# Kernel optimization log

Measured on AMD Instinct MI355X. Metric: run time of the kernel, lower is better.

The kernel has to match this reference:

```python
import jax, jax.numpy as jnp
import numpy as np

D = 1536          # d_model
H = 12            # n_heads // 2 for chunk attention
HD = D // H       # head dim = 128
MAXC = 256        # max_chunks
MAXLEN = 1024     # max_seq_length (size embedding table)
THRESH = 0.5      # boundary threshold (init value of the learned param)


def _gelu(v):
    return jax.nn.gelu(v, approximate=False)  # torch nn.GELU default (erf)


def _cos(a, b):
    # F.cosine_similarity with eps=1e-8
    na = jnp.maximum(jnp.linalg.norm(a, axis=-1), 1e-8)
    nb = jnp.maximum(jnp.linalg.norm(b, axis=-1), 1e-8)
    return jnp.sum(a * b, axis=-1) / (na * nb)


def _interp1d(y, L_out):
    # F.interpolate(mode='linear', align_corners=False) on [B, L_in] -> [B, L_out]
    L_in = y.shape[1]
    src = jnp.clip((jnp.arange(L_out, dtype=y.dtype) + 0.5) * (L_in / L_out) - 0.5, 0.0, L_in - 1)
    i0 = jnp.floor(src).astype(jnp.int32)
    i1 = jnp.minimum(i0 + 1, L_in - 1)
    w = src - i0.astype(y.dtype)
    return y[:, i0] * (1.0 - w) + y[:, i1] * w


def setup_inputs() -> dict:
    key = jax.random.key(0)
    ks = jax.random.split(key, 16)
    B, S = 4, 1024
    rn = lambda k, sh, s=0.02: jax.random.normal(k, sh, dtype=jnp.float32) * s
    return {
        'x': jax.random.normal(ks[0], (B, S, D), dtype=jnp.float32),
        'Wp': rn(ks[1], (D, D)), 'bp': jnp.zeros((D,), jnp.float32),
        'detW1': rn(ks[2], (3, D, 2 * D)), 'detb1': jnp.zeros((3, D), jnp.float32),
        'detW2': rn(ks[3], (3, D // 2, D)), 'detb2': jnp.zeros((3, D // 2), jnp.float32),
        'detW3': rn(ks[4], (3, D // 2)), 'detb3': jnp.zeros((3,), jnp.float32),
        'in_proj_w': rn(ks[5], (3 * D, D)), 'in_proj_b': jnp.zeros((3 * D,), jnp.float32),
        'out_w': rn(ks[6], (D, D)), 'out_b': jnp.zeros((D,), jnp.float32),
        'size_emb': jax.random.normal(ks[7], (MAXLEN, D), dtype=jnp.float32),
        'pos_enc': rn(ks[8], (1, MAXC, D)),
        'procW1': rn(ks[9], (2 * D, D)), 'procb1': jnp.zeros((2 * D,), jnp.float32),
        'procW2': rn(ks[10], (D, 2 * D)), 'procb2': jnp.zeros((D,), jnp.float32),
        'ln_g': jnp.ones((D,), jnp.float32), 'ln_b': jnp.zeros((D,), jnp.float32),
    }


def reference(x, Wp, bp, detW1, detb1, detW2, detb2, detW3, detb3,
              in_proj_w, in_proj_b, out_w, out_b, size_emb, pos_enc,
              procW1, procb1, procW2, procb2, ln_g, ln_b):
    B, S, d = x.shape
    # ---- DynamicSemanticChunker ----
    x_ling = x @ Wp.T + bp
    sims = []
    for scale in (1, 2, 4):
        xs = x_ling[:, ::scale]
        cs = _cos(xs[:, :-1], xs[:, 1:])           # [B, L-1]
        sims.append(_interp1d(cs, S - 1))           # [B, S-1]
    avg_sim = jnp.mean(jnp.stack(sims, 0), axis=0)
    base = 0.5 * (1.0 - avg_sim)
    bi = jnp.concatenate([x[:, :-1], x[:, 1:]], axis=-1)  # [B, S-1, 2d]
    h1 = _gelu(jnp.einsum('bsk,ndk->nbsd', bi, detW1) + detb1[:, None, None, :])
    h2 = _gelu(jnp.einsum('nbsd,nhd->nbsh', h1, detW2) + detb2[:, None, None, :])
    learned = jax.nn.sigmoid(jnp.einsum('nbsh,nh->nbs', h2, detW3) + detb3[:, None, None])
    avg_learned = jnp.mean(learned, axis=0)
    final = 0.6 * base + 0.4 * avg_learned
    boundaries = jnp.concatenate([jnp.ones((B, 1), x.dtype), final], axis=1)  # [B, S]
    # ---- EnhancedChunkLayer.create_chunks ----
    # contiguous ragged chunks == segments between boundary positions
    seg = jnp.cumsum((boundaries > THRESH).astype(jnp.int32), axis=1) - 1      # [B, S]
    # per-chunk MHA == full-seq attention with block-diagonal same-segment mask
    qkv = x @ in_proj_w.T + in_proj_b
    q, k, v = jnp.split(qkv, 3, axis=-1)
    q = q.reshape(B, S, H, HD)
    k = k.reshape(B, S, H, HD)
    v = v.reshape(B, S, H, HD)
    scores = jnp.einsum('bqhd,bkhd->bhqk', q, k) / np.sqrt(HD).astype(np.float32)
    same = (seg[:, None, :, None] == seg[:, None, None, :])                    # [B,1,S,S]
    scores = jnp.where(same, scores, jnp.asarray(-1e9, scores.dtype))
    attn = jax.nn.softmax(scores, axis=-1)
    ctx = jnp.einsum('bhqk,bkhd->bqhd', attn, v).reshape(B, S, d)
    attn_out = ctx @ out_w.T + out_b                                           # [B, S, d]
    # masked segment mean pooling; chunks with id >= MAXC are truncated away
    onehot = (seg[..., None] == jnp.arange(MAXC)).astype(x.dtype)              # [B,S,MAXC]
    sums = jnp.einsum('bsm,bsd->bmd', onehot, attn_out)
    counts = jnp.sum(onehot, axis=1)                                            # [B,MAXC]
    mean = sums / jnp.maximum(counts, 1.0)[..., None]
    clen = jnp.minimum(counts.astype(jnp.int32), MAXLEN - 1)
    sizes = size_emb[clen]                                                      # [B,MAXC,d]
    chunk = jnp.where(counts[..., None] > 0, mean + sizes, 0.0)                 # zero-pad empty
    # ---- pos encoding + chunk_processor (Linear->GELU->Linear->LayerNorm) ----
    chunk = chunk + pos_enc
    h = _gelu(chunk @ procW1.T + procb1)
    y = h @ procW2.T + procb2
    mu = jnp.mean(y, axis=-1, keepdims=True)
    var = jnp.var(y, axis=-1, keepdims=True)
    y = (y - mu) / jnp.sqrt(var + 1e-5) * ln_g + ln_b
    return y  # [B, MAXC, d]
```

## Files before the change

kernel.cpp:

```cpp
#include <hip/hip_runtime.h>
#include <hip/hip_bf16.h>
#include <math.h>

#define D_ 1536
#define S_ 1024
#define B_ 4
#define H_ 12
#define HD_ 128
#define MAXC_ 256

typedef __bf16 bf16x8_t __attribute__((ext_vector_type(8)));
typedef float f32x4_t __attribute__((ext_vector_type(4)));

__device__ __forceinline__ float gelu_f(float v) {
    return 0.5f * v * (1.0f + erff(v / 1.41421356237f));
}

__device__ __forceinline__ void split2(float a, __hip_bfloat16& h, __hip_bfloat16& l) {
    h = __float2bfloat16(a);
    l = __float2bfloat16(a - __bfloat162float(h));
}

template<int BM, int SPLITA, int SPLITB, int ACT, int OUT>
__global__ __launch_bounds__(256, 2)
void mfma3_gemm(const float* __restrict__ Af, const __hip_bfloat16* __restrict__ Ah,
                const __hip_bfloat16* __restrict__ Al,
                const float* __restrict__ Bf, const __hip_bfloat16* __restrict__ Bh,
                const __hip_bfloat16* __restrict__ Bl,
                const float* __restrict__ bias, int biasStride,
                float* __restrict__ Cf, __hip_bfloat16* __restrict__ Ch, __hip_bfloat16* __restrict__ Cl,
                const float* __restrict__ w3, float* __restrict__ lg,
                int K, int lda, int ldb, int ldc,
                long long aBound, long long azS, long long bzS, long long czS)
{
    __shared__ __align__(16) __hip_bfloat16 Ash[BM * 32], Asl[BM * 32];
    __shared__ __align__(16) __hip_bfloat16 Bsh[128 * 32], Bsl[128 * 32];
    const int z = blockIdx.z;
    const int bm = blockIdx.y * BM, bn = blockIdx.x * 128;
    const int tid = threadIdx.x, lane = tid & 63, wave = tid >> 6;
    const int wm = (BM == 128) ? (wave >> 1) : 0;
    const int wn = (BM == 128) ? (wave & 1) : wave;
    constexpr int NF = (BM == 128) ? 4 : 2;
    constexpr int WC = NF * 16;
    const int fr = lane & 15, kg = lane >> 4;
    f32x4_t acc[4][NF] = {};
    constexpr int RSH = (BM == 128) ? 1 : 2;
    constexpr int NBA = (BM == 128) ? 2 : 1;
    const int ar = tid >> RSH, akb = tid & ((1 << RSH) - 1);
    const int br = tid >> 1, bkb = tid & 1;

    for (int k0 = 0; k0 < K; k0 += 32) {
        #pragma unroll
        for (int j = 0; j < NBA; ++j) {
            int skg = akb * NBA + j;
            int blk = ar * 4 + (skg ^ ((ar >> 1) & 3));
            long long base = (long long)(bm + ar) * lda + azS * z + k0 + skg * 8;
            if (SPLITA) {
                float av[8];
                #pragma unroll
                for (int q = 0; q < 2; ++q) {
                    float4 v = make_float4(0.f, 0.f, 0.f, 0.f);
                    if (base + q * 4 + 4 <= aBound) v = *reinterpret_cast<const float4*>(&Af[base + q * 4]);
                    av[q * 4 + 0] = v.x; av[q * 4 + 1] = v.y; av[q * 4 + 2] = v.z; av[q * 4 + 3] = v.w;
                }
                __hip_bfloat16 hh[8], ll[8];
                #pragma unroll
                for (int q = 0; q < 8; ++q) split2(av[q], hh[q], ll[q]);
                *reinterpret_cast<bf16x8_t*>(&Ash[blk * 8]) = *reinterpret_cast<bf16x8_t*>(hh);
                *reinterpret_cast<bf16x8_t*>(&Asl[blk * 8]) = *reinterpret_cast<bf16x8_t*>(ll);
            } else {
                *reinterpret_cast<bf16x8_t*>(&Ash[blk * 8]) = *reinterpret_cast<const bf16x8_t*>(&Ah[base]);
                *reinterpret_cast<bf16x8_t*>(&Asl[blk * 8]) = *reinterpret_cast<const bf16x8_t*>(&Al[base]);
            }
        }
        #pragma unroll
        for (int j = 0; j < 2; ++j) {
            int skg = bkb * 2 + j;
            int blk = br * 4 + (skg ^ ((br >> 1) & 3));
            long long base = (long long)(bn + br) * ldb + bzS * z + k0 + skg * 8;
            if (SPLITB) {
                float av[8];
                #pragma unroll
                for (int q = 0; q < 2; ++q) {
                    float4 v = *reinterpret_cast<const float4*>(&Bf[base + q * 4]);
                    av[q * 4 + 0] = v.x; av[q * 4 + 1] = v.y; av[q * 4 + 2] = v.z; av[q * 4 + 3] = v.w;
                }
                __hip_bfloat16 hh[8], ll[8];
                #pragma unroll
                for (int q = 0; q < 8; ++q) split2(av[q], hh[q], ll[q]);
                *reinterpret_cast<bf16x8_t*>(&Bsh[blk * 8]) = *reinterpret_cast<bf16x8_t*>(hh);
                *reinterpret_cast<bf16x8_t*>(&Bsl[blk * 8]) = *reinterpret_cast<bf16x8_t*>(ll);
            } else {
                *reinterpret_cast<bf16x8_t*>(&Bsh[blk * 8]) = *reinterpret_cast<const bf16x8_t*>(&Bh[base]);
                *reinterpret_cast<bf16x8_t*>(&Bsl[blk * 8]) = *reinterpret_cast<const bf16x8_t*>(&Bl[base]);
            }
        }
        __syncthreads();
        bf16x8_t fah[4], fal[4], fbh[NF], fbl[NF];
        #pragma unroll
        for (int m = 0; m < 4; ++m) {
            int row = wm * 64 + m * 16 + fr;
            int blk = row * 4 + (kg ^ ((row >> 1) & 3));
            fah[m] = *reinterpret_cast<const bf16x8_t*>(&Ash[blk * 8]);
            fal[m] = *reinterpret_cast<const bf16x8_t*>(&Asl[blk * 8]);
        }
        #pragma unroll
        for (int n = 0; n < NF; ++n) {
            int row = wn * WC + n * 16 + fr;
            int blk = row * 4 + (kg ^ ((row >> 1) & 3));
            fbh[n] = *reinterpret_cast<const bf16x8_t*>(&Bsh[blk * 8]);
            fbl[n] = *reinterpret_cast<const bf16x8_t*>(&Bsl[blk * 8]);
        }
        #pragma unroll
        for (int m = 0; m < 4; ++m)
            #pragma unroll
            for (int n = 0; n < NF; ++n) {
                acc[m][n] = __builtin_amdgcn_mfma_f32_16x16x32_bf16(fah[m], fbh[n], acc[m][n], 0, 0, 0);
                acc[m][n] = __builtin_amdgcn_mfma_f32_16x16x32_bf16(fah[m], fbl[n], acc[m][n], 0, 0, 0);
                acc[m][n] = __builtin_amdgcn_mfma_f32_16x16x32_bf16(fal[m], fbh[n], acc[m][n], 0, 0, 0);
            }
        __syncthreads();
    }
    const int fq = lane >> 4;
    const float* bp_ = bias + (long long)biasStride * z;

    if constexpr (OUT == 2) {
        float psum[4][4] = {};
        #pragma unroll
        for (int n = 0; n < NF; ++n) {
            int col = bn + wn * WC + n * 16 + fr;
            float bv = bp_[col];
            float wv = w3[(long long)biasStride * z + col];
            #pragma unroll
            for (int m = 0; m < 4; ++m)
                #pragma unroll
                for (int r = 0; r < 4; ++r) {
                    float v = acc[m][n][r] + bv;
                    v = gelu_f(v);
                    psum[m][r] += v * wv;
                }
        }
        #pragma unroll
        for (int m = 0; m < 4; ++m)
            #pragma unroll
            for (int r = 0; r < 4; ++r) {
                float p = psum[m][r];
                p += __shfl_xor(p, 1);
                p += __shfl_xor(p, 2);
                p += __shfl_xor(p, 4);
                p += __shfl_xor(p, 8);
                if (fr == 0) {
                    int row = bm + wm * 64 + m * 16 + fq * 4 + r;
                    atomicAdd(&lg[czS * z + row], p);
                }
            }
        return;
    }

    #pragma unroll
    for (int n = 0; n < NF; ++n) {
        int col = bn + wn * WC + n * 16 + fr;
        float bv = bp_[col];
        #pragma unroll
        for (int m = 0; m < 4; ++m) {
            int row0 = bm + wm * 64 + m * 16 + fq * 4;
            #pragma unroll
            for (int r = 0; r < 4; ++r) {
                float v = acc[m][n][r] + bv;
                if (ACT == 1) v = gelu_f(v);
                long long ci = czS * z + (long long)(row0 + r) * ldc + col;
                if constexpr (OUT == 0) {
                    Cf[ci] = v;
                } else {
                    __hip_bfloat16 hh, ll;
                    split2(v, hh, ll);
                    Ch[ci] = hh; Cl[ci] = ll;
                }
            }
        }
    }
}

template<int ACT, int OUT_BF16>
__global__ __launch_bounds__(256)
void mfma_gemm(const __hip_bfloat16* __restrict__ A, const __hip_bfloat16* __restrict__ Bw,
               const float* __restrict__ bias, void* __restrict__ Cout,
               int M, int N, int K)
{
    __shared__ __align__(16) __hip_bfloat16 As[128 * 32];
    __shared__ __align__(16) __hip_bfloat16 Bs[128 * 32];
    const int tid = threadIdx.x;
    const int lane = tid & 63;
    const int wave = tid >> 6;
    const int wm = wave >> 1, wn = wave & 1;
    const int bm = blockIdx.y * 128, bn = blockIdx.x * 128;
    const int srow = tid >> 2;
    const int skg = tid & 3;
    const int fr = lane & 15, kg = lane >> 4;

    f32x4_t acc[4][4] = {};

    for (int k0 = 0; k0 < K; k0 += 32) {
        #pragma unroll
        for (int it = 0; it < 2; ++it) {
            int r = srow + it * 64;
            bf16x8_t va = *reinterpret_cast<const bf16x8_t*>(&A[(long long)(bm + r) * K + k0 + skg * 8]);
            bf16x8_t vb = *reinterpret_cast<const bf16x8_t*>(&Bw[(long long)(bn + r) * K + k0 + skg * 8]);
            int blk = r * 4 + (skg ^ ((r >> 1) & 3));
            *reinterpret_cast<bf16x8_t*>(&As[blk * 8]) = va;
            *reinterpret_cast<bf16x8_t*>(&Bs[blk * 8]) = vb;
        }
        __syncthreads();
        bf16x8_t af[4], bfr[4];
        #pragma unroll
        for (int m = 0; m < 4; ++m) {
            int row = wm * 64 + m * 16 + fr;
            af[m] = *reinterpret_cast<const bf16x8_t*>(&As[(row * 4 + (kg ^ ((row >> 1) & 3))) * 8]);
        }
        #pragma unroll
        for (int n = 0; n < 4; ++n) {
            int row = wn * 64 + n * 16 + fr;
            bfr[n] = *reinterpret_cast<const bf16x8_t*>(&Bs[(row * 4 + (kg ^ ((row >> 1) & 3))) * 8]);
        }
        #pragma unroll
        for (int m = 0; m < 4; ++m)
            #pragma unroll
            for (int n = 0; n < 4; ++n)
                acc[m][n] = __builtin_amdgcn_mfma_f32_16x16x32_bf16(af[m], bfr[n], acc[m][n], 0, 0, 0);
        __syncthreads();
    }
    const int fq = lane >> 4;
    #pragma unroll
    for (int n = 0; n < 4; ++n) {
        int col = bn + wn * 64 + n * 16 + fr;
        float bv = bias[col];
        #pragma unroll
        for (int m = 0; m < 4; ++m) {
            int row0 = bm + wm * 64 + m * 16 + fq * 4;
            #pragma unroll
            for (int r = 0; r < 4; ++r) {
                float v = acc[m][n][r] + bv;
                if (ACT == 1) v = gelu_f(v);
                if (OUT_BF16) ((__hip_bfloat16*)Cout)[(long long)(row0 + r) * N + col] = __float2bfloat16(v);
                else          ((float*)Cout)[(long long)(row0 + r) * N + col] = v;
            }
        }
    }
}

__global__ __launch_bounds__(256)
void f2b_kernel(const float* __restrict__ in, __hip_bfloat16* __restrict__ out, int n4)
{
    int i = blockIdx.x * 256 + threadIdx.x;
    if (i >= n4) return;
    float4 v = reinterpret_cast<const float4*>(in)[i];
    __hip_bfloat16 h[4] = { __float2bfloat16(v.x), __float2bfloat16(v.y),
                            __float2bfloat16(v.z), __float2bfloat16(v.w) };
    reinterpret_cast<short4*>(out)[i] = *reinterpret_cast<short4*>(h);
}

__global__ __launch_bounds__(256)
void split_kernel(const float* __restrict__ in, __hip_bfloat16* __restrict__ oh,
                  __hip_bfloat16* __restrict__ ol, int n4)
{
    int i = blockIdx.x * 256 + threadIdx.x;
    if (i >= n4) return;
    float4 v = reinterpret_cast<const float4*>(in)[i];
    __hip_bfloat16 h[4], l[4];
    split2(v.x, h[0], l[0]); split2(v.y, h[1], l[1]);
    split2(v.z, h[2], l[2]); split2(v.w, h[3], l[3]);
    reinterpret_cast<short4*>(oh)[i] = *reinterpret_cast<short4*>(h);
    reinterpret_cast<short4*>(ol)[i] = *reinterpret_cast<short4*>(l);
}

__global__ __launch_bounds__(64)
void cs_kernel(const float* __restrict__ xl, float* __restrict__ cs)
{
    int idx = blockIdx.x;
    int b = blockIdx.y;
    int sc, i, off;
    if (idx < 1023)      { sc = 1; i = idx;        off = 0;    }
    else if (idx < 1534) { sc = 2; i = idx - 1023; off = 1023; }
    else                 { sc = 4; i = idx - 1534; off = 1534; }
    const float* ra = xl + ((long long)b * S_ + (long long)i * sc) * D_;
    const float* rb = ra + (long long)sc * D_;
    int lane = threadIdx.x;
    float dp = 0.f, na = 0.f, nb = 0.f;
    for (int d = lane; d < D_; d += 64) {
        float a = ra[d], c = rb[d];
        dp += a * c; na += a * a; nb += c * c;
    }
    #pragma unroll
    for (int o = 32; o; o >>= 1) {
        dp += __shfl_down(dp, o);
        na += __shfl_down(na, o);
        nb += __shfl_down(nb, o);
    }
    if (lane == 0) {
        float den = fmaxf(sqrtf(na), 1e-8f) * fmaxf(sqrtf(nb), 1e-8f);
        cs[(long long)b * 1789 + off + i] = dp / den;
    }
}

__global__ void final_kernel(const float* __restrict__ cs, const float* __restrict__ logits,
                             const float* __restrict__ b3, float* __restrict__ fin)
{
    int g = blockIdx.x * blockDim.x + threadIdx.x;
    if (g >= B_ * 1023) return;
    int b = g / 1023, t = g % 1023;
    const float* c = cs + (long long)b * 1789;
    float v0 = c[t];
    const float r2 = (float)(511.0 / 1023.0);
    float src2 = fminf(fmaxf(((float)t + 0.5f) * r2 - 0.5f, 0.0f), 510.0f);
    int i0 = (int)floorf(src2);
    int i1 = min(i0 + 1, 510);
    float w2 = src2 - (float)i0;
    float v1 = c[1023 + i0] * (1.0f - w2) + c[1023 + i1] * w2;
    const float r4 = (float)(255.0 / 1023.0);
    float src4 = fminf(fmaxf(((float)t + 0.5f) * r4 - 0.5f, 0.0f), 254.0f);
    int j0 = (int)floorf(src4);
    int j1 = min(j0 + 1, 254);
    float w4 = src4 - (float)j0;
    float v2 = c[1534 + j0] * (1.0f - w4) + c[1534 + j1] * w4;
    float avg = ((v0 + v1) + v2) / 3.0f;
    float base = 0.5f * (1.0f - avg);
    int rr = b * 1024 + t;
    float l0 = 1.0f / (1.0f + expf(-(logits[0 * 4096 + rr] + b3[0])));
    float l1 = 1.0f / (1.0f + expf(-(logits[1 * 4096 + rr] + b3[1])));
    float l2 = 1.0f / (1.0f + expf(-(logits[2 * 4096 + rr] + b3[2])));
    float al = ((l0 + l1) + l2) / 3.0f;
    fin[g] = 0.6f * base + 0.4f * al;
}

__global__ __launch_bounds__(64)
void seg_kernel(const float* __restrict__ fin, int* __restrict__ seg)
{
    int b = blockIdx.x;
    int lane = threadIdx.x;
    int loc[16];
    int cnt = 0;
    #pragma unroll
    for (int i = 0; i < 16; ++i) {
        int t = lane * 16 + i;
        int v = (t >= 1 && fin[b * 1023 + t - 1] > 0.5f) ? 1 : 0;
        cnt += v;
        loc[i] = cnt;
    }
    int inc = cnt;
    #pragma unroll
    for (int o = 1; o < 64; o <<= 1) {
        int u = __shfl_up(inc, o);
        if (lane >= o) inc += u;
    }
    int ex = inc - cnt;
    #pragma unroll
    for (int i = 0; i < 16; ++i) {
        int t = lane * 16 + i;
        seg[b * S_ + t] = ex + loc[i];
    }
}

__global__ void segrange_kernel(const float* __restrict__ fin, const int* __restrict__ seg,
                                int* __restrict__ sstart, int* __restrict__ send,
                                int* __restrict__ cfirst, int* __restrict__ ccount)
{
    int gs = blockIdx.x * blockDim.x + threadIdx.x;
    if (gs >= B_ * S_) return;
    int b = gs / S_, s = gs % S_;
    const float* f = fin + b * 1023;
    int t = s;
    while (t > 0 && !(f[t - 1] > 0.5f)) --t;
    int e = s;
    while (e < 1023 && !(f[e] > 0.5f)) ++e;
    sstart[gs] = t;
    send[gs] = e + 1;
    if (s == t) {
        int m = seg[gs];
        if (m < MAXC_) { cfirst[b * MAXC_ + m] = t; ccount[b * MAXC_ + m] = e + 1 - t; }
    }
}

__global__ __launch_bounds__(64)
void attn_kernel(const __hip_bfloat16* __restrict__ qkv, const int* __restrict__ sstart,
                 const int* __restrict__ send, __hip_bfloat16* __restrict__ ctx)
{
    int gs = blockIdx.x;
    int h = blockIdx.y;
    int lane = threadIdx.x;
    int b = gs >> 10;
    const __hip_bfloat16* qrow = qkv + (long long)gs * 4608 + h * HD_;
    float q0 = __bfloat162float(qrow[lane]), q1 = __bfloat162float(qrow[lane + 64]);
    int st = sstart[gs], en = send[gs];
    float m = -INFINITY, l = 0.f, a0 = 0.f, a1 = 0.f;
    for (int t = st; t < en; ++t) {
        long long krow = ((long long)(b * S_ + t)) * 4608 + 1536 + h * HD_;
        float p = q0 * __bfloat162float(qkv[krow + lane]) + q1 * __bfloat162float(qkv[krow + lane + 64]);
        #pragma unroll
        for (int o = 32; o; o >>= 1) p += __shfl_xor(p, o);
        p = p / 11.3137084989847603904f;
        float nm = fmaxf(m, p);
        float scale = expf(m - nm);
        float w = expf(p - nm);
        long long vrow = ((long long)(b * S_ + t)) * 4608 + 3072 + h * HD_;
        l = l * scale + w;
        a0 = a0 * scale + w * __bfloat162float(qkv[vrow + lane]);
        a1 = a1 * scale + w * __bfloat162float(qkv[vrow + lane + 64]);
        m = nm;
    }
    float inv = 1.0f / l;
    ctx[(long long)gs * D_ + h * HD_ + lane] = __float2bfloat16(a0 * inv);
    ctx[(long long)gs * D_ + h * HD_ + lane + 64] = __float2bfloat16(a1 * inv);
}

__global__ __launch_bounds__(256)
void chunk_kernel(const float* __restrict__ attn_out, const int* __restrict__ cfirst,
                  const int* __restrict__ ccount, const float* __restrict__ size_emb,
                  const float* __restrict__ pos_enc, __hip_bfloat16* __restrict__ chunk)
{
    int m = blockIdx.x, b = blockIdx.y;
    int cnt = ccount[b * MAXC_ + m];
    for (int d = threadIdx.x; d < D_; d += 256) {
        float v;
        if (cnt > 0) {
            int first = cfirst[b * MAXC_ + m];
            float ssum = 0.f;
            for (int t = 0; t < cnt; ++t)
                ssum += attn_out[((long long)(b * S_ + first + t)) * D_ + d];
            float mean = ssum / (float)cnt;
            int clen = min(cnt, 1023);
            v = mean + size_emb[(long long)clen * D_ + d];
        } else {
            v = 0.f;
        }
        v += pos_enc[m * D_ + d];
        chunk[((long long)(b * MAXC_ + m)) * D_ + d] = __float2bfloat16(v);
    }
}

__global__ __launch_bounds__(256)
void ln_kernel(const float* __restrict__ y0, const float* __restrict__ g,
               const float* __restrict__ bb, float* __restrict__ out)
{
    int r = blockIdx.x;
    const float* row = y0 + (long long)r * D_;
    float loc[6];
    float s = 0.f;
    #pragma unroll
    for (int i = 0; i < 6; ++i) { loc[i] = row[threadIdx.x + i * 256]; s += loc[i]; }
    __shared__ float red[256];
    red[threadIdx.x] = s; __syncthreads();
    for (int o = 128; o; o >>= 1) { if (threadIdx.x < o) red[threadIdx.x] += red[threadIdx.x + o]; __syncthreads(); }
    float mu = red[0] / 1536.0f;
    __syncthreads();
    float s2 = 0.f;
    #pragma unroll
    for (int i = 0; i < 6; ++i) { float d = loc[i] - mu; s2 += d * d; }
    red[threadIdx.x] = s2; __syncthreads();
    for (int o = 128; o; o >>= 1) { if (threadIdx.x < o) red[threadIdx.x] += red[threadIdx.x + o]; __syncthreads(); }
    float var = red[0] / 1536.0f;
    float inv = 1.0f / sqrtf(var + 1e-5f);
    #pragma unroll
    for (int i = 0; i < 6; ++i) {
        int d = threadIdx.x + i * 256;
        out[(long long)r * D_ + d] = (loc[i] - mu) * inv * g[d] + bb[d];
    }
}

extern "C" void kernel_launch(void* const* d_in, const int* in_sizes, int n_in,
                              void* d_out, int out_size, void* d_ws, size_t ws_size,
                              hipStream_t stream)
{
    const float* x         = (const float*)d_in[0];
    const float* Wp        = (const float*)d_in[1];
    const float* bp        = (const float*)d_in[2];
    const float* detW1     = (const float*)d_in[3];
    const float* detb1     = (const float*)d_in[4];
    const float* detW2     = (const float*)d_in[5];
    const float* detb2     = (const float*)d_in[6];
    const float* detW3     = (const float*)d_in[7];
    const float* detb3     = (const float*)d_in[8];
    const float* in_proj_w = (const float*)d_in[9];
    const float* in_proj_b = (const float*)d_in[10];
    const float* out_w     = (const float*)d_in[11];
    const float* out_b     = (const float*)d_in[12];
    const float* size_emb  = (const float*)d_in[13];
    const float* pos_enc   = (const float*)d_in[14];
    const float* procW1    = (const float*)d_in[15];
    const float* procb1    = (const float*)d_in[16];
    const float* procW2    = (const float*)d_in[17];
    const float* procb2    = (const float*)d_in[18];
    const float* ln_g      = (const float*)d_in[19];
    const float* ln_b      = (const float*)d_in[20];
    float* out = (float*)d_out;

    const bool big = ws_size >= (size_t)192 * 1024 * 1024;

    char* ws = (char*)d_ws;
    float*          xlingf = (float*)(ws + 0);
    __hip_bfloat16* Wph    = (__hip_bfloat16*)(ws + 25165824);
    __hip_bfloat16* Wpl    = (__hip_bfloat16*)(ws + 29884416);
    __hip_bfloat16* h1h    = (__hip_bfloat16*)(ws + 0);
    __hip_bfloat16* h1l    = (__hip_bfloat16*)(ws + 37748736);
    __hip_bfloat16* W1h_s  = (__hip_bfloat16*)(ws + 75497472);
    __hip_bfloat16* W1l_s  = (__hip_bfloat16*)(ws + 94371840);
    __hip_bfloat16* W2h_s  = (__hip_bfloat16*)(ws + 75497472);
    __hip_bfloat16* W2l_s  = (__hip_bfloat16*)(ws + 82575360);
    __hip_bfloat16* xh     = (__hip_bfloat16*)(ws + 75497472);
    __hip_bfloat16* xl     = (__hip_bfloat16*)(ws + 88082432);
    __hip_bfloat16* W1h_b  = (__hip_bfloat16*)(ws + 125829120);
    __hip_bfloat16* W1l_b  = (__hip_bfloat16*)(ws + 154140672);
    __hip_bfloat16* W2h_b  = (__hip_bfloat16*)(ws + 125829120);
    __hip_bfloat16* W2l_b  = (__hip_bfloat16*)(ws + 132907008);
    __hip_bfloat16* xb_s       = (__hip_bfloat16*)(ws + 0);
    __hip_bfloat16* in_proj_wb = (__hip_bfloat16*)(ws + 12582912);
    __hip_bfloat16* qkvb       = (__hip_bfloat16*)(ws + 26738688);
    __hip_bfloat16* ctxb       = (__hip_bfloat16*)(ws + 64487424);
    __hip_bfloat16* out_wb     = (__hip_bfloat16*)(ws + 12582912);
    float*          attno      = (float*)(ws + 77070336);
    __hip_bfloat16* chunkb     = (__hip_bfloat16*)(ws + 0);
    __hip_bfloat16* procW1b    = (__hip_bfloat16*)(ws + 3145728);
    __hip_bfloat16* hmidb      = (__hip_bfloat16*)(ws + 12582912);
    __hip_bfloat16* procW2b    = (__hip_bfloat16*)(ws + 18874368);
    float*          y0         = (float*)(ws + 28311552);
    char* sm = ws + 113246208;
    float* csb    = (float*)(sm + 0);
    float* logits = (float*)(sm + 28672);
    float* fin    = (float*)(sm + 77824);
    int*   seg    = (int*)  (sm + 94208);
    int*   sstart = (int*)  (sm + 110592);
    int*   send   = (int*)  (sm + 126976);
    int*   cfirst = (int*)  (sm + 143360);
    int*   ccount = (int*)  (sm + 147456);

    const long long SLICE_W1 = 4718592LL;
    const long long SLICE_W2 = 1179648LL;
    const long long H1_Z     = 6291456LL;

    split_kernel<<<(2359296 / 4 + 255) / 256, 256, 0, stream>>>(Wp, Wph, Wpl, 2359296 / 4);
    if (big)
        split_kernel<<<(6291456 / 4 + 255) / 256, 256, 0, stream>>>(x, xh, xl, 6291456 / 4);

    if (big)
        mfma3_gemm<64, 0, 0, 0, 0><<<dim3(12, 64, 1), 256, 0, stream>>>(
            nullptr, xh, xl, nullptr, Wph, Wpl, bp, 0,
            xlingf, nullptr, nullptr, nullptr, nullptr,
            1536, 1536, 1536, 1536, 0LL, 0LL, 0LL, 0LL);
    else
        mfma3_gemm<64, 1, 0, 0, 0><<<dim3(12, 64, 1), 256, 0, stream>>>(
            x, nullptr, nullptr, nullptr, Wph, Wpl, bp, 0,
            xlingf, nullptr, nullptr, nullptr, nullptr,
            1536, 1536, 1536, 1536, 6291456LL, 0LL, 0LL, 0LL);
    cs_kernel<<<dim3(1789, 4), 64, 0, stream>>>(xlingf, csb);

    if (big) {
        split_kernel<<<(14155776 / 4 + 255) / 256, 256, 0, stream>>>(detW1, W1h_b, W1l_b, 14155776 / 4);
        mfma3_gemm<128, 0, 0, 1, 1><<<dim3(12, 32, 3), 256, 0, stream>>>(
            nullptr, xh, xl, nullptr, W1h_b, W1l_b, detb1, 1536,
            nullptr, h1h, h1l, nullptr, nullptr,
            3072, 1536, 3072, 1536, 0LL, 0LL, SLICE_W1, H1_Z);
    } else {
        split_kernel<<<(2 * 4718592 / 4 + 255) / 256, 256, 0, stream>>>(detW1, W1h_s, W1l_s, 2 * 4718592 / 4);
        mfma3_gemm<128, 1, 0, 1, 1><<<dim3(12, 32, 2), 256, 0, stream>>>(
            x, nullptr, nullptr, nullptr, W1h_s, W1l_s, detb1, 1536,
            nullptr, h1h, h1l, nullptr, nullptr,
            3072, 1536, 3072, 1536, 6291456LL, 0LL, SLICE_W1, H1_Z);
        split_kernel<<<(4718592 / 4 + 255) / 256, 256, 0, stream>>>(detW1 + 2 * SLICE_W1, W1h_s, W1l_s, 4718592 / 4);
        mfma3_gemm<64, 1, 0, 1, 1><<<dim3(12, 64, 1), 256, 0, stream>>>(
            x, nullptr, nullptr, nullptr, W1h_s, W1l_s, detb1 + 2 * 1536, 1536,
            nullptr, h1h + 2 * H1_Z, h1l + 2 * H1_Z, nullptr, nullptr,
            3072, 1536, 3072, 1536, 6291456LL, 0LL, 0LL, 0LL);
    }

    __hip_bfloat16* W2h = big ? W2h_b : W2h_s;
    __hip_bfloat16* W2l = big ? W2l_b : W2l_s;
    split_kernel<<<(3538944 / 4 + 255) / 256, 256, 0, stream>>>(detW2, W2h, W2l, 3538944 / 4);
    hipMemsetAsync(logits, 0, 3 * 4096 * sizeof(float), stream);
    mfma3_gemm<128, 0, 0, 1, 2><<<dim3(6, 32, 3), 256, 0, stream>>>(
        nullptr, h1h, h1l, nullptr, W2h, W2l, detb2, 768,
        nullptr, nullptr, nullptr, detW3, logits,
        1536, 1536, 1536, 768, 0LL, H1_Z, SLICE_W2, 4096LL);

    final_kernel<<<16, 256, 0, stream>>>(csb, logits, detb3, fin);
    seg_kernel<<<4, 64, 0, stream>>>(fin, seg);
    hipMemsetAsync(ccount, 0, B_ * MAXC_ * sizeof(int), stream);
    segrange_kernel<<<16, 256, 0, stream>>>(fin, seg, sstart, send, cfirst, ccount);

    const __hip_bfloat16* xbf;
    if (big) {
        xbf = xh;
    } else {
        f2b_kernel<<<(4096 * 1536 / 4 + 255) / 256, 256, 0, stream>>>(x, xb_s, 4096 * 1536 / 4);
        xbf = xb_s;
    }
    f2b_kernel<<<(4608 * 1536 / 4 + 255) / 256, 256, 0, stream>>>(in_proj_w, in_proj_wb, 4608 * 1536 / 4);
    mfma_gemm<0, 1><<<dim3(36, 32), 256, 0, stream>>>(xbf, in_proj_wb, in_proj_b, qkvb, 4096, 4608, 1536);

    attn_kernel<<<dim3(4096, 12), 64, 0, stream>>>(qkvb, sstart, send, ctxb);

    f2b_kernel<<<(1536 * 1536 / 4 + 255) / 256, 256, 0, stream>>>(out_w, out_wb, 1536 * 1536 / 4);
    mfma_gemm<0, 0><<<dim3(12, 32), 256, 0, stream>>>(ctxb, out_wb, out_b, attno, 4096, 1536, 1536);

    chunk_kernel<<<dim3(256, 4), 256, 0, stream>>>(attno, cfirst, ccount, size_emb, pos_enc, chunkb);

    f2b_kernel<<<(3072 * 1536 / 4 + 255) / 256, 256, 0, stream>>>(procW1, procW1b, 3072 * 1536 / 4);
    mfma_gemm<1, 1><<<dim3(24, 8), 256, 0, stream>>>(chunkb, procW1b, procb1, hmidb, 1024, 3072, 1536);
    f2b_kernel<<<(1536 * 3072 / 4 + 255) / 256, 256, 0, stream>>>(procW2, procW2b, 1536 * 3072 / 4);
    mfma_gemm<0, 0><<<dim3(12, 8), 256, 0, stream>>>(hmidb, procW2b, procb2, y0, 1024, 1536, 3072);

    ln_kernel<<<1024, 256, 0, stream>>>(y0, ln_g, ln_b, out);
}
```

Measured before the change: 1.287 ms.

## Prefetch next K tile into registers and swizzle blocks across XCDs in GEMMs

Both MFMA GEMM kernels now load the next K-slice from global memory into registers while the current slice is being multiplied, then write it to shared memory after a barrier. This hides global-load latency behind the MFMA work. Block indices are also remapped so that neighbouring tiles land on the same XCD, which should improve L2 reuse. The projection GEMM in the big path switches from 64-row to 128-row tiles. The cost is more registers per thread and an extra barrier per iteration.

```diff
diff --git a/kernel.cpp b/kernel.cpp
--- a/kernel.cpp
+++ b/kernel.cpp
@@ -19,6 +19,16 @@
 __device__ __forceinline__ void split2(float a, __hip_bfloat16& h, __hip_bfloat16& l) {
     h = __float2bfloat16(a);
     l = __float2bfloat16(a - __bfloat162float(h));
+}
+
+__device__ __forceinline__ void xcd_swizzle(int& bx, int& by, int gx, int gy) {
+    int nwg = gx * gy;
+    int orig = by * gx + bx;
+    int xcd = orig & 7;
+    int q = nwg >> 3, r = nwg & 7;
+    int wg = (xcd < r ? xcd * (q + 1) : r * (q + 1) + (xcd - r) * q) + (orig >> 3);
+    bx = wg % gx;
+    by = wg / gx;
 }
 
 template<int BM, int SPLITA, int SPLITB, int ACT, int OUT>
@@ -36,7 +46,9 @@
     __shared__ __align__(16) __hip_bfloat16 Ash[BM * 32], Asl[BM * 32];
     __shared__ __align__(16) __hip_bfloat16 Bsh[128 * 32], Bsl[128 * 32];
     const int z = blockIdx.z;
-    const int bm = blockIdx.y * BM, bn = blockIdx.x * 128;
+    int bxi = blockIdx.x, byi = blockIdx.y;
+    xcd_swizzle(bxi, byi, gridDim.x, gridDim.y);
+    const int bm = byi * BM, bn = bxi * 128;
     const int tid = threadIdx.x, lane = tid & 63, wave = tid >> 6;
     const int wm = (BM == 128) ? (wave >> 1) : 0;
     const int wn = (BM == 128) ? (wave & 1) : wave;
@@ -49,53 +61,88 @@
     const int ar = tid >> RSH, akb = tid & ((1 << RSH) - 1);
     const int br = tid >> 1, bkb = tid & 1;
 
-    for (int k0 = 0; k0 < K; k0 += 32) {
+    bf16x8_t rAh[NBA], rAl[NBA], rBh[2], rBl[2];
+    float4 rAf[NBA][2], rBf[2][2];
+
+    auto load_tile = [&](int k0) {
         #pragma unroll
         for (int j = 0; j < NBA; ++j) {
             int skg = akb * NBA + j;
-            int blk = ar * 4 + (skg ^ ((ar >> 1) & 3));
             long long base = (long long)(bm + ar) * lda + azS * z + k0 + skg * 8;
             if (SPLITA) {
-                float av[8];
                 #pragma unroll
                 for (int q = 0; q < 2; ++q) {
                     float4 v = make_float4(0.f, 0.f, 0.f, 0.f);
                     if (base + q * 4 + 4 <= aBound) v = *reinterpret_cast<const float4*>(&Af[base + q * 4]);
-                    av[q * 4 + 0] = v.x; av[q * 4 + 1] = v.y; av[q * 4 + 2] = v.z; av[q * 4 + 3] = v.w;
+                    rAf[j][q] = v;
                 }
+            } else {
+                rAh[j] = *reinterpret_cast<const bf16x8_t*>(&Ah[base]);
+                rAl[j] = *reinterpret_cast<const bf16x8_t*>(&Al[base]);
+            }
+        }
+        #pragma unroll
+        for (int j = 0; j < 2; ++j) {
+            int skg = bkb * 2 + j;
+            long long base = (long long)(bn + br) * ldb + bzS * z + k0 + skg * 8;
+            if (SPLITB) {
+                #pragma unroll
+                for (int q = 0; q < 2; ++q)
+                    rBf[j][q] = *reinterpret_cast<const float4*>(&Bf[base + q * 4]);
+            } else {
+                rBh[j] = *reinterpret_cast<const bf16x8_t*>(&Bh[base]);
+                rBl[j] = *reinterpret_cast<const bf16x8_t*>(&Bl[base]);
+            }
+        }
+    };
+
+    auto write_tile = [&]() {
+        #pragma unroll
+        for (int j = 0; j < NBA; ++j) {
+            int skg = akb * NBA + j;
+            int blk = ar * 4 + (skg ^ ((ar >> 1) & 3));
+            if (SPLITA) {
+                float av[8];
+                *reinterpret_cast<float4*>(&av[0]) = rAf[j][0];
+                *reinterpret_cast<float4*>(&av[4]) = rAf[j][1];
                 __hip_bfloat16 hh[8], ll[8];
                 #pragma unroll
                 for (int q = 0; q < 8; ++q) split2(av[q], hh[q], ll[q]);
                 *reinterpret_cast<bf16x8_t*>(&Ash[blk * 8]) = *reinterpret_cast<bf16x8_t*>(hh);
                 *reinterpret_cast<bf16x8_t*>(&Asl[blk * 8]) = *reinterpret_cast<bf16x8_t*>(ll);
             } else {
-                *reinterpret_cast<bf16x8_t*>(&Ash[blk * 8]) = *reinterpret_cast<const bf16x8_t*>(&Ah[base]);
-                *reinterpret_cast<bf16x8_t*>(&Asl[blk * 8]) = *reinterpret_cast<const bf16x8_t*>(&Al[base]);
+                *reinterpret_cast<bf16x8_t*>(&Ash[blk * 8]) = rAh[j];
+                *reinterpret_cast<bf16x8_t*>(&Asl[blk * 8]) = rAl[j];
             }
         }
         #pragma unroll
         for (int j = 0; j < 2; ++j) {
             int skg = bkb * 2 + j;
             int blk = br * 4 + (skg ^ ((br >> 1) & 3));
-            long long base = (long long)(bn + br) * ldb + bzS * z + k0 + skg * 8;
             if (SPLITB) {
                 float av[8];
-                #pragma unroll
-                for (int q = 0; q < 2; ++q) {
-                    float4 v = *reinterpret_cast<const float4*>(&Bf[base + q * 4]);
-                    av[q * 4 + 0] = v.x; av[q * 4 + 1] = v.y; av[q * 4 + 2] = v.z; av[q * 4 + 3] = v.w;
-                }
+                *reinterpret_cast<float4*>(&av[0]) = rBf[j][0];
+                *reinterpret_cast<float4*>(&av[4]) = rBf[j][1];
                 __hip_bfloat16 hh[8], ll[8];
                 #pragma unroll
                 for (int q = 0; q < 8; ++q) split2(av[q], hh[q], ll[q]);
                 *reinterpret_cast<bf16x8_t*>(&Bsh[blk * 8]) = *reinterpret_cast<bf16x8_t*>(hh);
                 *reinterpret_cast<bf16x8_t*>(&Bsl[blk * 8]) = *reinterpret_cast<bf16x8_t*>(ll);
             } else {
-                *reinterpret_cast<bf16x8_t*>(&Bsh[blk * 8]) = *reinterpret_cast<const bf16x8_t*>(&Bh[base]);
-                *reinterpret_cast<bf16x8_t*>(&Bsl[blk * 8]) = *reinterpret_cast<const bf16x8_t*>(&Bl[base]);
-            }
-        }
-        __syncthreads();
+                *reinterpret_cast<bf16x8_t*>(&Bsh[blk * 8]) = rBh[j];
+                *reinterpret_cast<bf16x8_t*>(&Bsl[blk * 8]) = rBl[j];
+            }
+        }
+    };
+
+    load_tile(0);
+    write_tile();
+    __syncthreads();
+
+    for (int k0 = 0; k0 < K; k0 += 32) {
+        const bool has_next = (k0 + 32) < K;
+        if (has_next) load_tile(k0 + 32);
+
         bf16x8_t fah[4], fal[4], fbh[NF], fbl[NF];
         #pragma unroll
         for (int m = 0; m < 4; ++m) {
@@ -119,8 +166,14 @@
                 acc[m][n] = __builtin_amdgcn_mfma_f32_16x16x32_bf16(fah[m], fbl[n], acc[m][n], 0, 0, 0);
                 acc[m][n] = __builtin_amdgcn_mfma_f32_16x16x32_bf16(fal[m], fbh[n], acc[m][n], 0, 0, 0);
             }
-        __syncthreads();
-    }
+
+        if (has_next) {
+            __syncthreads();
+            write_tile();
+            __syncthreads();
+        }
+    }
+
     const int fq = lane >> 4;
     const float* bp_ = bias + (long long)biasStride * z;
 
@@ -193,24 +246,42 @@
     const int lane = tid & 63;
     const int wave = tid >> 6;
     const int wm = wave >> 1, wn = wave & 1;
-    const int bm = blockIdx.y * 128, bn = blockIdx.x * 128;
+    int bxi = blockIdx.x, byi = blockIdx.y;
+    xcd_swizzle(bxi, byi, gridDim.x, gridDim.y);
+    const int bm = byi * 128, bn = bxi * 128;
     const int srow = tid >> 2;
     const int skg = tid & 3;
     const int fr = lane & 15, kg = lane >> 4;
 
     f32x4_t acc[4][4] = {};
-
-    for (int k0 = 0; k0 < K; k0 += 32) {
+    bf16x8_t rA[2], rB[2];
+
+    auto load_tile = [&](int k0) {
         #pragma unroll
         for (int it = 0; it < 2; ++it) {
             int r = srow + it * 64;
-            bf16x8_t va = *reinterpret_cast<const bf16x8_t*>(&A[(long long)(bm + r) * K + k0 + skg * 8]);
-            bf16x8_t vb = *reinterpret_cast<const bf16x8_t*>(&Bw[(long long)(bn + r) * K + k0 + skg * 8]);
+            rA[it] = *reinterpret_cast<const bf16x8_t*>(&A[(long long)(bm + r) * K + k0 + skg * 8]);
+            rB[it] = *reinterpret_cast<const bf16x8_t*>(&Bw[(long long)(bn + r) * K + k0 + skg * 8]);
+        }
+    };
+    auto write_tile = [&]() {
+        #pragma unroll
+        for (int it = 0; it < 2; ++it) {
+            int r = srow + it * 64;
             int blk = r * 4 + (skg ^ ((r >> 1) & 3));
-            *reinterpret_cast<bf16x8_t*>(&As[blk * 8]) = va;
-            *reinterpret_cast<bf16x8_t*>(&Bs[blk * 8]) = vb;
-        }
-        __syncthreads();
+            *reinterpret_cast<bf16x8_t*>(&As[blk * 8]) = rA[it];
+            *reinterpret_cast<bf16x8_t*>(&Bs[blk * 8]) = rB[it];
+        }
+    };
+
+    load_tile(0);
+    write_tile();
+    __syncthreads();
+
+    for (int k0 = 0; k0 < K; k0 += 32) {
+        const bool has_next = (k0 + 32) < K;
+        if (has_next) load_tile(k0 + 32);
+
         bf16x8_t af[4], bfr[4];
         #pragma unroll
         for (int m = 0; m < 4; ++m) {
@@ -227,7 +298,12 @@
             #pragma unroll
             for (int n = 0; n < 4; ++n)
                 acc[m][n] = __builtin_amdgcn_mfma_f32_16x16x32_bf16(af[m], bfr[n], acc[m][n], 0, 0, 0);
-        __syncthreads();
+
+        if (has_next) {
+            __syncthreads();
+            write_tile();
+            __syncthreads();
+        }
     }
     const int fq = lane >> 4;
     #pragma unroll
@@ -541,7 +617,7 @@
         split_kernel<<<(6291456 / 4 + 255) / 256, 256, 0, stream>>>(x, xh, xl, 6291456 / 4);
 
     if (big)
-        mfma3_gemm<64, 0, 0, 0, 0><<<dim3(12, 64, 1), 256, 0, stream>>>(
+        mfma3_gemm<128, 0, 0, 0, 0><<<dim3(12, 32, 1), 256, 0, stream>>>(
             nullptr, xh, xl, nullptr, Wph, Wpl, bp, 0,
             xlingf, nullptr, nullptr, nullptr, nullptr,
             1536, 1536, 1536, 1536, 0LL, 0LL, 0LL, 0LL);
```

New measurement: 1.110 ms. 13.7% less time.
